# Kernel optimization log

Measured on AMD Instinct MI355X. Metric: run time of the kernel, lower is better.

Reference implementation:

```python
import jax, jax.numpy as jnp
import numpy as np

DIM_V = 512
NUM_HEADS = 8
LN_EPS = 1e-5


def _layernorm(x):
    # LayerNorm over last dim, no affine (simplified_layer_norm=True)
    mu = jnp.mean(x, axis=-1, keepdims=True)
    var = jnp.mean(jnp.square(x - mu), axis=-1, keepdims=True)
    return (x - mu) * jax.lax.rsqrt(var + LN_EPS)


def setup_inputs() -> dict:
    key = jax.random.key(0)
    ks = jax.random.split(key, 12)
    B, Nq, Nk, dQ, dK, dV = 16, 1024, 1024, 512, 512, DIM_V
    s = 0.02
    return {
        "Q": jax.random.normal(ks[0], (B, Nq, dQ), jnp.float32),
        "K": jax.random.normal(ks[1], (B, Nk, dK), jnp.float32),
        "Wq": jax.random.normal(ks[2], (dQ, dV), jnp.float32) * s,
        "bq": jnp.zeros((dV,), jnp.float32),
        "Wk": jax.random.normal(ks[3], (dK, dV), jnp.float32) * s,
        "bk": jnp.zeros((dV,), jnp.float32),
        "Wv": jax.random.normal(ks[4], (dK, dV), jnp.float32) * s,
        "bv": jnp.zeros((dV,), jnp.float32),
        "Wo": jax.random.normal(ks[5], (dV, dV), jnp.float32) * s,
        "bo": jnp.zeros((dV,), jnp.float32),
    }


def reference(Q, K, Wq, bq, Wk, bk, Wv, bv, Wo, bo):
    H = NUM_HEADS
    dh = DIM_V // H
    q = Q @ Wq + bq            # [B, Nq, dV]
    k = K @ Wk + bk            # [B, Nk, dV]
    v = K @ Wv + bv            # [B, Nk, dV]
    B, Nq, _ = q.shape
    Nk = k.shape[1]
    qh = q.reshape(B, Nq, H, dh)
    kh = k.reshape(B, Nk, H, dh)
    vh = v.reshape(B, Nk, H, dh)
    # NOTE: faithful to source — scale by sqrt(dim_V), not sqrt(head_dim)
    scores = jnp.einsum('bqhd,bkhd->bhqk', qh, kh) / jnp.sqrt(jnp.asarray(DIM_V, q.dtype))
    A = jax.nn.softmax(scores, axis=-1)                    # [B, H, Nq, Nk]
    attn = jnp.einsum('bhqk,bkhd->bqhd', A, vh).reshape(B, Nq, DIM_V)
    O = q + attn               # residual with projected Q
    O = _layernorm(O)          # ln0 (no affine)
    O = O + jax.nn.gelu(O @ Wo + bo, approximate=False)
    O = _layernorm(O)          # ln1 (no affine)
    return O
```

## Files before the change

### kernel.cpp

```cpp
#include <hip/hip_runtime.h>
#include <hip/hip_bf16.h>
#include <math.h>

typedef __bf16 bf16;
typedef __bf16 bf16x8 __attribute__((ext_vector_type(8)));
typedef float  f32x4  __attribute__((ext_vector_type(4)));

#define MFMA16(a,b,c) __builtin_amdgcn_mfma_f32_16x16x32_bf16((a),(b),(c),0,0,0)
#define ATT_SCALE 0.0441941738241592f

__device__ __forceinline__ void async16p(const void* g, void* l) {
    __builtin_amdgcn_global_load_lds((const __attribute__((address_space(1))) void*)g,
                                     (__attribute__((address_space(3))) void*)l,
                                     16, 0, 0);
}

__global__ __launch_bounds__(256) void prep_w_kernel(
    const float* __restrict__ Wq, const float* __restrict__ Wk,
    const float* __restrict__ Wv, const float* __restrict__ Wo,
    bf16* __restrict__ WqT, bf16* __restrict__ WkT,
    bf16* __restrict__ WvT, bf16* __restrict__ WoT)
{
    __shared__ float tile[32][33];
    const int bx = blockIdx.x;
    const float* W; bf16* T;
    switch (bx >> 8) {
      case 0: W=Wq; T=WqT; break;
      case 1: W=Wk; T=WkT; break;
      case 2: W=Wv; T=WvT; break;
      default: W=Wo; T=WoT; break;
    }
    const int rest = bx & 255;
    const int k0 = (rest & 15) * 32, n0 = (rest >> 4) * 32;
    const int tx = threadIdx.x & 31, ty = threadIdx.x >> 5;
    #pragma unroll
    for (int i=0;i<32;i+=8)
        tile[ty+i][tx] = W[(size_t)(k0+ty+i)*512 + n0+tx];
    __syncthreads();
    #pragma unroll
    for (int i=0;i<32;i+=8)
        T[(size_t)(n0+ty+i)*512 + k0+tx] = (bf16)tile[tx][ty+i];
}

__global__ __launch_bounds__(256, 3) void gemm_qkv_kernel(
    const float* __restrict__ Qf, const float* __restrict__ Kf,
    const bf16* __restrict__ WqT, const bf16* __restrict__ WkT,
    const bf16* __restrict__ WvT,
    const float* __restrict__ bq, const float* __restrict__ bk,
    const float* __restrict__ bv,
    bf16* __restrict__ qbb, bf16* __restrict__ kbb, bf16* __restrict__ vT)
{
    __shared__ __align__(16) char smem[24576];
    float* As32 = (float*)smem;
    bf16*  Bs   = (bf16*)(smem + 16384);
    bf16*  Lt   = (bf16*)smem;

    const int z = blockIdx.z;
    const float* A  = (z == 0) ? Qf  : Kf;
    const bf16*  BT = (z == 0) ? WqT : (z == 1) ? WkT : WvT;
    const float* bb = (z == 0) ? bq  : (z == 1) ? bk  : bv;

    const int m0 = blockIdx.x * 128, n0 = blockIdx.y * 128;
    const int tid = threadIdx.x;
    const int lane = tid & 63, wave = tid >> 6;
    const int qd = lane >> 4, lr = lane & 15;
    const int wm = (wave & 1) * 64, wn = (wave >> 1) * 64;

    const float* gA = A + (size_t)(m0 + (tid>>3))*512 + (((tid&7)^((tid>>3)&7))*4);
    float* lA = As32 + wave*256;
    const bf16* gB = BT + (size_t)(n0 + (tid>>2))*512 + (((tid&3)^((tid>>2)&3))*8);
    bf16* lB = Bs + wave*512;

    f32x4 acc[4][4];
    #pragma unroll
    for (int i=0;i<4;i++)
      #pragma unroll
      for (int j=0;j<4;j++) acc[i][j] = (f32x4){0,0,0,0};

    for (int k0 = 0; k0 < 512; k0 += 32) {
        __syncthreads();
        #pragma unroll
        for (int i=0;i<4;i++)
            async16p(gA + k0 + (size_t)i*32*512, lA + i*1024);
        async16p(gB + k0,          lB);
        async16p(gB + k0 + 64*512, lB + 2048);
        __syncthreads();
        bf16x8 af[4], bfr[4];
        #pragma unroll
        for (int mi=0;mi<4;mi++) {
            int row = wm + mi*16 + lr;
            f32x4 f0 = *(f32x4*)(As32 + row*32 + (((qd*2  )^(lr&7))*4));
            f32x4 f1 = *(f32x4*)(As32 + row*32 + (((qd*2+1)^(lr&7))*4));
            bf16x8 a;
            a[0]=(bf16)f0[0]; a[1]=(bf16)f0[1]; a[2]=(bf16)f0[2]; a[3]=(bf16)f0[3];
            a[4]=(bf16)f1[0]; a[5]=(bf16)f1[1]; a[6]=(bf16)f1[2]; a[7]=(bf16)f1[3];
            af[mi] = a;
        }
        #pragma unroll
        for (int ni=0;ni<4;ni++)
            bfr[ni] = *(bf16x8*)(Bs + (wn+ni*16+lr)*32 + ((qd^(lr&3))*8));
        #pragma unroll
        for (int mi=0;mi<4;mi++)
          #pragma unroll
          for (int ni=0;ni<4;ni++)
            acc[mi][ni] = MFMA16(af[mi], bfr[ni], acc[mi][ni]);
    }

    if (z < 2) {
        bf16* C = (z == 0) ? qbb : kbb;
        #pragma unroll
        for (int ni=0;ni<4;ni++) {
            int n = n0 + wn + ni*16 + lr;
            float bv0 = bb[n];
            #pragma unroll
            for (int mi=0;mi<4;mi++) {
                int mb = m0 + wm + mi*16 + qd*4;
                #pragma unroll
                for (int r=0;r<4;r++)
                    C[(size_t)(mb+r)*512 + n] = (bf16)(acc[mi][ni][r] + bv0);
            }
        }
    } else {
        const int b = m0 >> 10, tok0 = m0 & 1023;
        const int row = tid >> 2, ch = tid & 3;
        #pragma unroll
        for (int half = 0; half < 2; ++half) {
            __syncthreads();
            if ((wn >> 6) == half) {
                #pragma unroll
                for (int ni=0;ni<4;ni++) {
                    int nl = ni*16 + lr;
                    float bvv = bb[n0 + half*64 + nl];
                    #pragma unroll
                    for (int mi=0;mi<4;mi++)
                      #pragma unroll
                      for (int r=0;r<4;r++) {
                        int col = wm + mi*16 + qd*4 + r;
                        Lt[nl*128 + ((((col>>3)^(nl&7))<<3) | (col&7))]
                            = (bf16)(acc[mi][ni][r] + bvv);
                      }
                }
            }
            __syncthreads();
            const int h = (n0 >> 6) + half;
            bf16* dst = vT + ((size_t)((b*8 + h)*64 + row))*1024 + tok0 + ch*32;
            #pragma unroll
            for (int s=0;s<4;s++) {
                int g = (ch*4 + s) ^ (row & 7);
                *(uint4*)(dst + s*8) = *(uint4*)(Lt + row*128 + g*8);
            }
        }
    }
}

__global__ __launch_bounds__(256, 4) void attn_kernel(
    const bf16* __restrict__ qb, const bf16* __restrict__ kb,
    const bf16* __restrict__ vT, bf16* __restrict__ attnb)
{
    const int qt = blockIdx.x, h = blockIdx.y, b = blockIdx.z;
    const int tid = threadIdx.x, lane = tid & 63, wave = tid >> 6;
    const int qd = lane >> 4, lr = lane & 15;
    const int q0 = qt*128 + wave*32;

    __shared__ bf16 Ks[64][72];
    __shared__ bf16 Vs[64][72];
    __shared__ bf16 Pl[4][32][72];

    bf16x8 aq[2][2];
    #pragma unroll
    for (int mi=0;mi<2;mi++) {
        const bf16* qrow = qb + ((size_t)(b*1024 + q0 + mi*16 + lr))*512 + h*64;
        aq[mi][0] = *(const bf16x8*)(qrow + qd*8);
        aq[mi][1] = *(const bf16x8*)(qrow + 32 + qd*8);
    }

    const int srow = tid >> 2;
    const int scol = (tid & 3) * 16;
    const bf16* kgp = kb + ((size_t)(b*1024 + srow))*512 + h*64 + scol;
    const bf16* vgp = vT + ((size_t)((b*8 + h)*64 + srow))*1024 + scol;

    uint4 k0r = *(const uint4*)(kgp);
    uint4 k1r = *(const uint4*)(kgp + 8);
    uint4 v0r = *(const uint4*)(vgp);
    uint4 v1r = *(const uint4*)(vgp + 8);

    f32x4 acc[2][4];
    #pragma unroll
    for (int mi=0;mi<2;mi++)
      #pragma unroll
      for (int ni=0;ni<4;ni++) acc[mi][ni] = (f32x4){0,0,0,0};
    float l[2][4] = {{0,0,0,0},{0,0,0,0}};

    for (int t=0; t<16; ++t) {
        __syncthreads();
        *(uint4*)(&Ks[srow][scol])   = k0r;
        *(uint4*)(&Ks[srow][scol+8]) = k1r;
        *(uint4*)(&Vs[srow][scol])   = v0r;
        *(uint4*)(&Vs[srow][scol+8]) = v1r;
        __syncthreads();
        if (t < 15) {
            const size_t kk = (size_t)(t+1)*64;
            k0r = *(const uint4*)(kgp + kk*512);
            k1r = *(const uint4*)(kgp + kk*512 + 8);
            v0r = *(const uint4*)(vgp + kk);
            v1r = *(const uint4*)(vgp + kk + 8);
        }

        f32x4 s[2][4];
        #pragma unroll
        for (int mi=0;mi<2;mi++)
          #pragma unroll
          for (int ni=0;ni<4;ni++) s[mi][ni] = (f32x4){0,0,0,0};
        #pragma unroll
        for (int ni=0;ni<4;ni++) {
            bf16x8 b0 = *(bf16x8*)(&Ks[ni*16+lr][qd*8]);
            bf16x8 b1 = *(bf16x8*)(&Ks[ni*16+lr][32+qd*8]);
            #pragma unroll
            for (int mi=0;mi<2;mi++) {
                s[mi][ni] = MFMA16(aq[mi][0], b0, s[mi][ni]);
                s[mi][ni] = MFMA16(aq[mi][1], b1, s[mi][ni]);
            }
        }
        #pragma unroll
        for (int mi=0;mi<2;mi++)
          #pragma unroll
          for (int ni=0;ni<4;ni++)
            #pragma unroll
            for (int r=0;r<4;r++) {
                float pv = __expf(s[mi][ni][r] * ATT_SCALE);
                s[mi][ni][r] = pv;
                l[mi][r] += pv;
            }
        #pragma unroll
        for (int mi=0;mi<2;mi++)
          #pragma unroll
          for (int ni=0;ni<4;ni++)
            #pragma unroll
            for (int r=0;r<4;r++)
                Pl[wave][mi*16 + qd*4 + r][ni*16 + lr] = (bf16)s[mi][ni][r];
        bf16x8 ap[2][2];
        #pragma unroll
        for (int mi=0;mi<2;mi++) {
            ap[mi][0] = *(bf16x8*)(&Pl[wave][mi*16+lr][qd*8]);
            ap[mi][1] = *(bf16x8*)(&Pl[wave][mi*16+lr][32+qd*8]);
        }
        #pragma unroll
        for (int ni=0;ni<4;ni++) {
            bf16x8 v0 = *(bf16x8*)(&Vs[ni*16+lr][qd*8]);
            bf16x8 v1 = *(bf16x8*)(&Vs[ni*16+lr][32+qd*8]);
            #pragma unroll
            for (int mi=0;mi<2;mi++) {
                acc[mi][ni] = MFMA16(ap[mi][0], v0, acc[mi][ni]);
                acc[mi][ni] = MFMA16(ap[mi][1], v1, acc[mi][ni]);
            }
        }
    }

    #pragma unroll
    for (int off=1; off<16; off<<=1)
      #pragma unroll
      for (int mi=0;mi<2;mi++)
        #pragma unroll
        for (int r=0;r<4;r++) l[mi][r] += __shfl_xor(l[mi][r], off);

    #pragma unroll
    for (int mi=0;mi<2;mi++) {
        float inv[4];
        #pragma unroll
        for (int r=0;r<4;r++) inv[r] = 1.f / l[mi][r];
        #pragma unroll
        for (int ni=0;ni<4;ni++)
          #pragma unroll
          for (int r=0;r<4;r++)
            Pl[wave][qd*4+r][ni*16+lr] = (bf16)(acc[mi][ni][r] * inv[r]);
        bf16x8 oA = *(bf16x8*)(&Pl[wave][lr][qd*8]);
        bf16x8 oB = *(bf16x8*)(&Pl[wave][lr][32+qd*8]);
        bf16x8 rA, rB;
        #pragma unroll
        for (int j=0;j<8;j++) {
            rA[j] = (bf16)((float)oA[j] + (float)aq[mi][0][j]);
            rB[j] = (bf16)((float)oB[j] + (float)aq[mi][1][j]);
        }
        bf16* dst = attnb + ((size_t)(b*1024 + q0 + mi*16 + lr))*512 + h*64;
        *(bf16x8*)(dst + qd*8)      = rA;
        *(bf16x8*)(dst + 32 + qd*8) = rB;
    }
}

__global__ __launch_bounds__(256) void ln0_kernel(
    const bf16* __restrict__ attnb, bf16* __restrict__ Obf)
{
    const int wave = threadIdx.x >> 6, lane = threadIdx.x & 63;
    const int row = blockIdx.x*4 + wave;
    const size_t base = (size_t)row*512 + lane*8;
    bf16x8 av = *(const bf16x8*)(attnb + base);
    float x[8];
    #pragma unroll
    for (int i=0;i<8;i++) x[i] = (float)av[i];
    float s1 = 0.f, s2 = 0.f;
    #pragma unroll
    for (int i=0;i<8;i++){ s1 += x[i]; s2 += x[i]*x[i]; }
    #pragma unroll
    for (int off=1; off<64; off<<=1) { s1 += __shfl_xor(s1, off); s2 += __shfl_xor(s2, off); }
    float mu  = s1 * (1.f/512.f);
    float var = s2 * (1.f/512.f) - mu*mu;
    float rstd = rsqrtf(var + 1e-5f);
    bf16x8 ob;
    #pragma unroll
    for (int i=0;i<8;i++) ob[i] = (bf16)((x[i]-mu)*rstd);
    *(bf16x8*)(Obf + base) = ob;
}

__device__ __forceinline__ void gemm_core(
    const bf16* __restrict__ A, const bf16* __restrict__ BT,
    int m0, int n0, char* smem, f32x4 (&acc)[4][4])
{
    bf16* As = (bf16*)smem;
    bf16* Bs = (bf16*)(smem + 16384);
    const int tid = threadIdx.x;
    const int lane = tid & 63, wave = tid >> 6;
    const int qd = lane >> 4, lr = lane & 15;
    const int wm = (wave & 1) * 64, wn = (wave >> 1) * 64;

    const int srow = tid >> 3;
    const int sgr  = ((tid & 7) ^ (srow & 7)) * 8;
    const bf16* gA = A  + (size_t)(m0 + srow)*512 + sgr;
    const bf16* gB = BT + (size_t)(n0 + srow)*512 + sgr;
    bf16* lA = As + wave*512;
    bf16* lB = Bs + wave*512;

    for (int k0 = 0; k0 < 512; k0 += 64) {
        __syncthreads();
        #pragma unroll
        for (int i=0;i<4;i++) {
            async16p(gA + k0 + (size_t)i*32*512, lA + i*2048);
            async16p(gB + k0 + (size_t)i*32*512, lB + i*2048);
        }
        __syncthreads();
        #pragma unroll
        for (int half=0; half<2; ++half) {
            bf16x8 af[4], bfr[4];
            #pragma unroll
            for (int mi=0;mi<4;mi++) {
                int row = wm + mi*16 + lr;
                af[mi] = *(bf16x8*)(As + row*64 + (((half*4+qd)^(lr&7))*8));
            }
            #pragma unroll
            for (int ni=0;ni<4;ni++) {
                int row = wn + ni*16 + lr;
                bfr[ni] = *(bf16x8*)(Bs + row*64 + (((half*4+qd)^(lr&7))*8));
            }
            #pragma unroll
            for (int mi=0;mi<4;mi++)
              #pragma unroll
              for (int ni=0;ni<4;ni++)
                acc[mi][ni] = MFMA16(af[mi], bfr[ni], acc[mi][ni]);
        }
    }
}

__global__ __launch_bounds__(256, 4) void gemm_o_kernel(
    const bf16* __restrict__ Obf, const bf16* __restrict__ WoT,
    const float* __restrict__ bo, bf16* __restrict__ xb)
{
    __shared__ __align__(16) char smem[32768];
    const int m0 = blockIdx.x * 128, n0 = blockIdx.y * 128;
    const int tid = threadIdx.x;
    const int lane = tid & 63, wave = tid >> 6;
    const int qd = lane >> 4, lr = lane & 15;
    const int wm = (wave & 1) * 64, wn = (wave >> 1) * 64;

    f32x4 acc[4][4];
    #pragma unroll
    for (int i=0;i<4;i++)
      #pragma unroll
      for (int j=0;j<4;j++) acc[i][j] = (f32x4){0,0,0,0};

    gemm_core(Obf, WoT, m0, n0, smem, acc);

    #pragma unroll
    for (int ni=0;ni<4;ni++) {
        int n = n0 + wn + ni*16 + lr;
        float bv = bo[n];
        #pragma unroll
        for (int mi=0;mi<4;mi++) {
            int mb = m0 + wm + mi*16 + qd*4;
            #pragma unroll
            for (int r=0;r<4;r++) {
                float g = acc[mi][ni][r] + bv;
                float gelu = 0.5f * g * (1.f + erff(g * 0.70710678118654752f));
                size_t idx = (size_t)(mb+r)*512 + n;
                xb[idx] = (bf16)((float)Obf[idx] + gelu);
            }
        }
    }
}

__global__ __launch_bounds__(256) void ln1_kernel(
    const bf16* __restrict__ xb, float* __restrict__ out)
{
    const int wave = threadIdx.x >> 6, lane = threadIdx.x & 63;
    const int row = blockIdx.x*4 + wave;
    const size_t base = (size_t)row*512 + lane*8;
    bf16x8 xv = *(const bf16x8*)(xb + base);
    float x[8];
    #pragma unroll
    for (int i=0;i<8;i++) x[i] = (float)xv[i];
    float s1 = 0.f, s2 = 0.f;
    #pragma unroll
    for (int i=0;i<8;i++){ s1 += x[i]; s2 += x[i]*x[i]; }
    #pragma unroll
    for (int off=1; off<64; off<<=1) { s1 += __shfl_xor(s1, off); s2 += __shfl_xor(s2, off); }
    float mu  = s1 * (1.f/512.f);
    float var = s2 * (1.f/512.f) - mu*mu;
    float rstd = rsqrtf(var + 1e-5f);
    float4 o0 = {(x[0]-mu)*rstd,(x[1]-mu)*rstd,(x[2]-mu)*rstd,(x[3]-mu)*rstd};
    float4 o1 = {(x[4]-mu)*rstd,(x[5]-mu)*rstd,(x[6]-mu)*rstd,(x[7]-mu)*rstd};
    *(float4*)(out + base)     = o0;
    *(float4*)(out + base + 4) = o1;
}

extern "C" void kernel_launch(void* const* d_in, const int* in_sizes, int n_in,
                              void* d_out, int out_size, void* d_ws, size_t ws_size,
                              hipStream_t stream)
{
    (void)in_sizes; (void)n_in; (void)out_size; (void)ws_size;
    const float* Q  = (const float*)d_in[0];
    const float* K  = (const float*)d_in[1];
    const float* Wq = (const float*)d_in[2];
    const float* bq = (const float*)d_in[3];
    const float* Wk = (const float*)d_in[4];
    const float* bk = (const float*)d_in[5];
    const float* Wv = (const float*)d_in[6];
    const float* bv = (const float*)d_in[7];
    const float* Wo = (const float*)d_in[8];
    const float* bo = (const float*)d_in[9];
    float* out = (float*)d_out;

    const size_t nTok = (size_t)16*1024*512;
    char* p = (char*)d_ws;
    auto alloc = [&](size_t bytes)->char* {
        char* r = p; p += (bytes + 255) & ~(size_t)255; return r;
    };
    bf16* WqT   = (bf16*)alloc(512*512*2);
    bf16* WkT   = (bf16*)alloc(512*512*2);
    bf16* WvT   = (bf16*)alloc(512*512*2);
    bf16* WoT   = (bf16*)alloc(512*512*2);
    bf16* qbb   = (bf16*)alloc(nTok*2);
    bf16* kbb   = (bf16*)alloc(nTok*2);
    bf16* vT    = (bf16*)alloc(nTok*2);
    bf16* attnb = (bf16*)alloc(nTok*2);
    bf16* Obf   = (bf16*)alloc(nTok*2);
    bf16* xb    = (bf16*)alloc(nTok*2);

    prep_w_kernel<<<1024, 256, 0, stream>>>(Wq, Wk, Wv, Wo, WqT, WkT, WvT, WoT);
    gemm_qkv_kernel<<<dim3(128,4,3), 256, 0, stream>>>(Q, K, WqT, WkT, WvT,
                                                       bq, bk, bv, qbb, kbb, vT);
    attn_kernel<<<dim3(8,8,16), 256, 0, stream>>>(qbb, kbb, vT, attnb);
    ln0_kernel<<<4096, 256, 0, stream>>>(attnb, Obf);
    gemm_o_kernel<<<dim3(128,4), 256, 0, stream>>>(Obf, WoT, bo, xb);
    ln1_kernel<<<4096, 256, 0, stream>>>(xb, out);
}
```

Before: 271.4 us.

## Double-buffer LDS tiles in QKV and output-projection GEMMs with async prefetch

Both GEMM main loops now use two LDS buffers. The next k-tile is issued through global_load_lds while the current tile feeds the MFMAs, with explicit vmcnt waits replacing the load-then-sync pattern. The gemm_core k-step shrinks from 64 to 32, and both kernels get a new XOR swizzle for the 32-wide bf16 rows. The QKV kernel's shared memory doubles to 48KB, which may limit how many blocks fit per CU under launch_bounds(256,3).

After: 268.1 us. Within noise of the previous version (-1.2%).

```diff
diff --git a/kernel.cpp b/kernel.cpp
--- a/kernel.cpp
+++ b/kernel.cpp
@@ -50,9 +50,9 @@
     const float* __restrict__ bv,
     bf16* __restrict__ qbb, bf16* __restrict__ kbb, bf16* __restrict__ vT)
 {
-    __shared__ __align__(16) char smem[24576];
+    __shared__ __align__(16) char smem[49152];
     float* As32 = (float*)smem;
-    bf16*  Bs   = (bf16*)(smem + 16384);
+    bf16*  Bs   = (bf16*)(smem + 32768);
     bf16*  Lt   = (bf16*)smem;
 
     const int z = blockIdx.z;
@@ -67,9 +67,7 @@
     const int wm = (wave & 1) * 64, wn = (wave >> 1) * 64;
 
     const float* gA = A + (size_t)(m0 + (tid>>3))*512 + (((tid&7)^((tid>>3)&7))*4);
-    float* lA = As32 + wave*256;
-    const bf16* gB = BT + (size_t)(n0 + (tid>>2))*512 + (((tid&3)^((tid>>2)&3))*8);
-    bf16* lB = Bs + wave*512;
+    const bf16*  gB = BT + (size_t)(n0 + (tid>>2))*512 + (((tid&3)^((tid>>3)&3))*8);
 
     f32x4 acc[4][4];
     #pragma unroll
@@ -77,20 +75,37 @@
       #pragma unroll
       for (int j=0;j<4;j++) acc[i][j] = (f32x4){0,0,0,0};
 
-    for (int k0 = 0; k0 < 512; k0 += 32) {
-        __syncthreads();
+    auto stage = [&](int buf, int k0) {
+        float* lA = As32 + buf*4096 + wave*256;
+        bf16*  lB = Bs   + buf*4096 + wave*512;
         #pragma unroll
         for (int i=0;i<4;i++)
             async16p(gA + k0 + (size_t)i*32*512, lA + i*1024);
-        async16p(gB + k0,          lB);
-        async16p(gB + k0 + 64*512, lB + 2048);
-        __syncthreads();
+        async16p(gB + k0,                  lB);
+        async16p(gB + k0 + (size_t)64*512, lB + 2048);
+    };
+
+    stage(0, 0);
+    for (int t = 0; t < 16; ++t) {
+        const int cur = t & 1;
+        __builtin_amdgcn_sched_barrier(0);
+        __builtin_amdgcn_s_barrier();
+        if (t < 15) {
+            stage(cur ^ 1, (t+1)*32);
+            asm volatile("s_waitcnt vmcnt(6)" ::: "memory");
+        } else {
+            asm volatile("s_waitcnt vmcnt(0)" ::: "memory");
+        }
+        __builtin_amdgcn_s_barrier();
+
+        const float* Ab = As32 + cur*4096;
+        const bf16*  Bb = Bs   + cur*4096;
         bf16x8 af[4], bfr[4];
         #pragma unroll
         for (int mi=0;mi<4;mi++) {
             int row = wm + mi*16 + lr;
-            f32x4 f0 = *(f32x4*)(As32 + row*32 + (((qd*2  )^(lr&7))*4));
-            f32x4 f1 = *(f32x4*)(As32 + row*32 + (((qd*2+1)^(lr&7))*4));
+            f32x4 f0 = *(f32x4*)(Ab + row*32 + (((qd*2  )^(lr&7))*4));
+            f32x4 f1 = *(f32x4*)(Ab + row*32 + (((qd*2+1)^(lr&7))*4));
             bf16x8 a;
             a[0]=(bf16)f0[0]; a[1]=(bf16)f0[1]; a[2]=(bf16)f0[2]; a[3]=(bf16)f0[3];
             a[4]=(bf16)f1[0]; a[5]=(bf16)f1[1]; a[6]=(bf16)f1[2]; a[7]=(bf16)f1[3];
@@ -98,7 +113,7 @@
         }
         #pragma unroll
         for (int ni=0;ni<4;ni++)
-            bfr[ni] = *(bf16x8*)(Bs + (wn+ni*16+lr)*32 + ((qd^(lr&3))*8));
+            bfr[ni] = *(bf16x8*)(Bb + (wn+ni*16+lr)*32 + ((qd^((lr>>1)&3))*8));
         #pragma unroll
         for (int mi=0;mi<4;mi++)
           #pragma unroll
@@ -322,40 +337,47 @@
     const int qd = lane >> 4, lr = lane & 15;
     const int wm = (wave & 1) * 64, wn = (wave >> 1) * 64;
 
-    const int srow = tid >> 3;
-    const int sgr  = ((tid & 7) ^ (srow & 7)) * 8;
+    const int srow = tid >> 2;
+    const int sgr  = ((tid & 3) ^ ((tid >> 3) & 3)) * 8;
     const bf16* gA = A  + (size_t)(m0 + srow)*512 + sgr;
     const bf16* gB = BT + (size_t)(n0 + srow)*512 + sgr;
-    bf16* lA = As + wave*512;
-    bf16* lB = Bs + wave*512;
-
-    for (int k0 = 0; k0 < 512; k0 += 64) {
-        __syncthreads();
-        #pragma unroll
-        for (int i=0;i<4;i++) {
-            async16p(gA + k0 + (size_t)i*32*512, lA + i*2048);
-            async16p(gB + k0 + (size_t)i*32*512, lB + i*2048);
-        }
-        __syncthreads();
-        #pragma unroll
-        for (int half=0; half<2; ++half) {
-            bf16x8 af[4], bfr[4];
-            #pragma unroll
-            for (int mi=0;mi<4;mi++) {
-                int row = wm + mi*16 + lr;
-                af[mi] = *(bf16x8*)(As + row*64 + (((half*4+qd)^(lr&7))*8));
-            }
-            #pragma unroll
-            for (int ni=0;ni<4;ni++) {
-                int row = wn + ni*16 + lr;
-                bfr[ni] = *(bf16x8*)(Bs + row*64 + (((half*4+qd)^(lr&7))*8));
-            }
-            #pragma unroll
-            for (int mi=0;mi<4;mi++)
-              #pragma unroll
-              for (int ni=0;ni<4;ni++)
-                acc[mi][ni] = MFMA16(af[mi], bfr[ni], acc[mi][ni]);
-        }
+
+    auto stage = [&](int buf, int k0) {
+        bf16* lA = As + buf*4096 + wave*512;
+        bf16* lB = Bs + buf*4096 + wave*512;
+        async16p(gA + k0,                  lA);
+        async16p(gA + k0 + (size_t)64*512, lA + 2048);
+        async16p(gB + k0,                  lB);
+        async16p(gB + k0 + (size_t)64*512, lB + 2048);
+    };
+
+    stage(0, 0);
+    for (int t = 0; t < 16; ++t) {
+        const int cur = t & 1;
+        __builtin_amdgcn_sched_barrier(0);
+        __builtin_amdgcn_s_barrier();
+        if (t < 15) {
+            stage(cur ^ 1, (t+1)*32);
+            asm volatile("s_waitcnt vmcnt(4)" ::: "memory");
+        } else {
+            asm volatile("s_waitcnt vmcnt(0)" ::: "memory");
+        }
+        __builtin_amdgcn_s_barrier();
+
+        const bf16* Ab = As + cur*4096;
+        const bf16* Bb = Bs + cur*4096;
+        bf16x8 af[4], bfr[4];
+        #pragma unroll
+        for (int mi=0;mi<4;mi++)
+            af[mi] = *(bf16x8*)(Ab + (wm+mi*16+lr)*32 + ((qd^((lr>>1)&3))*8));
+        #pragma unroll
+        for (int ni=0;ni<4;ni++)
+            bfr[ni] = *(bf16x8*)(Bb + (wn+ni*16+lr)*32 + ((qd^((lr>>1)&3))*8));
+        #pragma unroll
+        for (int mi=0;mi<4;mi++)
+          #pragma unroll
+          for (int ni=0;ni<4;ni++)
+            acc[mi][ni] = MFMA16(af[mi], bfr[ni], acc[mi][ni]);
     }
 }
 
```
